# Optimization experiments

Measured on AMD Instinct MI355X. Metric: run time of the kernel, lower is better.

## Reference

```python
import jax, jax.numpy as jnp
import numpy as np

B, G, C = 32, 512, 768
BG = B * G
H = 12              # MHA heads
MID, H1, N1 = 12, 6, 128   # Attention1 mid dim, heads, fixed block size
AD = 16             # adapter bottleneck
FF = 4 * C
NCLUST = 2048       # 3d grid cells
GRID = 196
D1 = B * GRID       # 1d scatter dim_size
NVIEW = 6
SCALE_FACTOR = 0.5
COEF_PRO = 0.3
EPS = 1e-5


def layernorm(x, g, b):
    m = x.mean(-1, keepdims=True)
    v = x.var(-1, keepdims=True)
    return (x - m) / jnp.sqrt(v + EPS) * g + b


def quick_gelu(x):
    return x * jax.nn.sigmoid(1.702 * x)


def bn_gelu(x, g, b):
    # BatchNorm1d in training mode (batch statistics, biased var) + exact GELU
    m = x.mean(0)
    v = x.var(0)
    y = (x - m) / jnp.sqrt(v + EPS) * g + b
    return jax.nn.gelu(y, approximate=False)


def seg_max_mean(feat, idx, nseg):
    # segment_csr(sorted feat, ptr) == segment reduce over cluster ids; empty segments -> 0
    cnt = jax.ops.segment_sum(jnp.ones((feat.shape[0], 1), feat.dtype), idx, nseg)
    smax = jnp.where(cnt > 0, jax.ops.segment_max(feat, idx, nseg), 0.0)
    smean = jax.ops.segment_sum(feat, idx, nseg) / jnp.maximum(cnt, 1.0)
    return smax, smean


def setup_inputs() -> dict:
    key = jax.random.key(0)
    ks = iter(jax.random.split(key, 40))
    r = lambda shape, s=0.02: jax.random.normal(next(ks), shape, jnp.float32) * s
    return {
        "x": jax.random.normal(next(ks), (B, G + 1, C), jnp.float32),
        "ln1_g": jnp.ones((C,)), "ln1_b": jnp.zeros((C,)),
        "ln2_g": jnp.ones((C,)), "ln2_b": jnp.zeros((C,)),
        "Wqkv": r((3 * C, C)), "bqkv": jnp.zeros((3 * C,)),
        "Wo": r((C, C)), "bo": jnp.zeros((C,)),
        "Wfc": r((FF, C)), "bfc": jnp.zeros((FF,)),
        "Wproj": r((C, FF)), "bproj": jnp.zeros((C,)),
        "Wa1": r((AD, C)), "ba1": jnp.zeros((AD,)),
        "Wa2": r((C, AD)), "ba2": jnp.zeros((C,)),
        "bn3d_g": jnp.ones((C,)), "bn3d_b": jnp.zeros((C,)),
        "bn1d_g": jnp.ones((NVIEW, C)), "bn1d_b": jnp.zeros((NVIEW, C)),
        "n3_g": jnp.ones((NVIEW, C)), "n3_b": jnp.zeros((NVIEW, C)),
        "a1_qkv_w": r((NVIEW, 3 * MID, C)), "a1_qkv_b": jnp.zeros((NVIEW, 3 * MID)),
        "a1_proj_w": r((NVIEW, C, MID)), "a1_proj_b": jnp.zeros((NVIEW, C)),
        "cluster": jax.random.randint(next(ks), (BG,), 0, NCLUST),
        "flat_grid_index": jax.random.randint(next(ks), (NVIEW, BG), 0, D1),
        "mask": jax.random.randint(next(ks), (NVIEW, BG // N1, N1, N1), 0, 2).astype(bool),
    }


def reference(x, ln1_g, ln1_b, ln2_g, ln2_b, Wqkv, bqkv, Wo, bo, Wfc, bfc,
              Wproj, bproj, Wa1, ba1, Wa2, ba2, bn3d_g, bn3d_b, bn1d_g, bn1d_b,
              n3_g, n3_b, a1_qkv_w, a1_qkv_b, a1_proj_w, a1_proj_b,
              cluster, flat_grid_index, mask):
    hd = C // H
    # --- multi-head self-attention over tokens + residual ---
    y = layernorm(x, ln1_g, ln1_b)
    qkv = y @ Wqkv.T + bqkv                          # [B, S, 3C]
    q, k, v = jnp.split(qkv, 3, axis=-1)
    heads = lambda t: t.reshape(B, G + 1, H, hd).transpose(0, 2, 1, 3)
    q, k, v = heads(q), heads(k), heads(v)
    attn = jax.nn.softmax(jnp.einsum('bhqd,bhkd->bhqk', q, k) / jnp.sqrt(jnp.float32(hd)), axis=-1)
    o = jnp.einsum('bhqk,bhkd->bhqd', attn, v).transpose(0, 2, 1, 3).reshape(B, G + 1, C)
    x = x + o @ Wo.T + bo
    # --- MLP (QuickGELU) + scaled adapter ---
    y = layernorm(x, ln2_g, ln2_b)
    x_ffn = quick_gelu(y @ Wfc.T + bfc) @ Wproj.T + bproj
    adapt = quick_gelu(x_ffn @ Wa1.T + ba1) @ Wa2.T + ba2
    x = x + x_ffn + SCALE_FACTOR * adapt
    cls_x = x[:, :1]
    xt = x[:, 1:]                                    # [B, G, C]
    feat = xt.reshape(BG, C)
    # --- 3d cluster pooling: segment max+mean -> BN+GELU -> gather back ---
    fmax, fmean = seg_max_mean(feat, cluster, NCLUST)
    x_3d = bn_gelu(fmax + fmean, bn3d_g, bn3d_b)[cluster].reshape(B, G, C)
    # --- per-view local masked attention + 1d grid scatter pooling (vmapped) ---
    def view_branch(n3g, n3b, qkvw, qkvb, projw, projb, bng, bnb, idx, msk):
        z = layernorm(feat, n3g, n3b)
        qkv1 = (z @ qkvw.T + qkvb).reshape(BG // N1, N1, 3, H1, MID // H1).transpose(2, 0, 3, 1, 4)
        q1, k1, v1 = qkv1[0], qkv1[1], qkv1[2]       # [Bn, H1, N1, hd1]
        a = jnp.einsum('bhqd,bhkd->bhqk', q1, k1) * (MID ** -0.5)
        a = a + jnp.where(msk, -100000.0, 0.0)[:, None]  # mask broadcast over heads
        a = jax.nn.softmax(a, axis=-1)
        o1 = jnp.einsum('bhqk,bhkd->bhqd', a, v1).transpose(0, 2, 1, 3).reshape(BG, MID)
        flat = o1 @ projw.T + projb + feat
        smax, smean = seg_max_mean(flat, idx, D1)
        return bn_gelu(smax + smean, bng, bnb)[idx].reshape(B, G, C)
    pos = jax.vmap(view_branch)(n3_g, n3_b, a1_qkv_w, a1_qkv_b, a1_proj_w, a1_proj_b,
                                bn1d_g, bn1d_b, flat_grid_index, mask)   # [6, B, G, C]
    # --- cosine-similarity-weighted fusion of the 6 views against x_3d ---
    def cossim(a, b):
        na = jnp.maximum(jnp.linalg.norm(a, axis=-1), 1e-8)
        nb = jnp.maximum(jnp.linalg.norm(b, axis=-1), 1e-8)
        return (a * b).sum(-1) / (na * nb)
    sims = (jax.vmap(lambda p: cossim(p, x_3d))(pos) + 1.0) / 2.0        # [6, B, G]
    sims = sims / sims.sum(0, keepdims=True)
    x_sup = (pos * sims[..., None]).sum(0)                               # [B, G, C]
    xt = xt + COEF_PRO * x_sup
    return jnp.concatenate([cls_x, xt], axis=1)
```

## Files before the change

kernel.cpp:

```cpp
#include <hip/hip_runtime.h>
#include <hip/hip_bf16.h>
#include <math.h>

typedef unsigned int u32;
typedef __hip_bfloat16 bf16;
typedef __attribute__((ext_vector_type(8))) short bh8;
typedef __attribute__((ext_vector_type(4))) float fx4;
typedef __attribute__((ext_vector_type(2))) unsigned int u32x2;
typedef __attribute__((ext_vector_type(4))) unsigned int u32x4;

#define CDIM   768
#define BATCH  32
#define SEQ    513
#define NT     (BATCH*SEQ)
#define NR     16384
#define NHEAD  12
#define HD     64
#define FFDIM  3072
#define NCLUST 2048
#define D1SEG  6272
#define NVIEW  6
#define MIDD   12
#define H1N    6
#define N1V    128
#define NB1    128
#define CHROWS 8208

#define A_FS      ((size_t)0)
#define B_FS      ((size_t)6303744)
#define X1_FS     ((size_t)25214976)
#define AH_FS     ((size_t)31518720)
#define D_FS      ((size_t)31781376)
#define DTOT_FS   9640064
#define X3D_FS    ((size_t)(D_FS + DTOT_FS))
#define BNV_FS    (X3D_FS + 1572864)
#define STATM_FS  (BNV_FS + 14450688)
#define STATR_FS  (STATM_FS + 768)
#define DI_CNT    (D_FS)
#define DI_BASE   (D_FS + 6272)
#define DI_CUR    (D_FS + 12544)
#define DI_ORD    (D_FS + 18816)
#define DW_FS     (D_FS + 40960)
#define DWV_FS    (D_FS + 3600000)

__device__ inline float b2f(bf16 v){ return __bfloat162float(v); }
__device__ inline float ldv(const float* p, size_t i){ return p[i]; }
__device__ inline float ldv(const bf16*  p, size_t i){ return __bfloat162float(p[i]); }
__device__ inline void  stv(float* p, size_t i, float v){ p[i] = v; }
__device__ inline void  stv(bf16*  p, size_t i, float v){ p[i] = __float2bfloat16(v); }
__device__ inline short f2bs(float f){ bf16 h = __float2bfloat16(f); return *(short*)&h; }
__device__ inline void gload_lds16(const bf16* g, short* l){
    __builtin_amdgcn_global_load_lds((const __attribute__((address_space(1))) void*)g,
                                     (__attribute__((address_space(3))) void*)l, 16, 0, 0);
}
__device__ inline u32x2 ds_tr16(unsigned a){
    u32x2 d;
    asm volatile("ds_read_b64_tr_b16 %0, %1" : "=v"(d) : "v"(a));
    return d;
}
__device__ inline unsigned cvtpk_bf16(float lo, float hi){
    unsigned r;
    asm("v_cvt_pk_bf16_f32 %0, %1, %2" : "=v"(r) : "v"(lo), "v"(hi));
    return r;
}


__global__ __launch_bounds__(256) void k_zero(float* p, int n){
    for (int i = blockIdx.x*256 + threadIdx.x; i < n; i += gridDim.x*256) p[i] = 0.0f;
}

__global__ __launch_bounds__(256) void k_f2b5(const float* __restrict__ a0, bf16* __restrict__ b0, int n0,
                                              const float* __restrict__ a1, bf16* __restrict__ b1, int n1,
                                              const float* __restrict__ a2, bf16* __restrict__ b2, int n2,
                                              const float* __restrict__ a3, bf16* __restrict__ b3, int n3,
                                              const float* __restrict__ a4, bf16* __restrict__ b4, int n4){
    int i0 = blockIdx.x*256 + threadIdx.x, st = gridDim.x*256;
    for (int i=i0; i<n0; i+=st) b0[i] = __float2bfloat16(a0[i]);
    for (int i=i0; i<n1; i+=st) b1[i] = __float2bfloat16(a1[i]);
    for (int i=i0; i<n2; i+=st) b2[i] = __float2bfloat16(a2[i]);
    for (int i=i0; i<n3; i+=st) b3[i] = __float2bfloat16(a3[i]);
    for (int i=i0; i<n4; i+=st) b4[i] = __float2bfloat16(a4[i]);
}

template<typename TI>
__global__ __launch_bounds__(256) void k_ln(const TI* __restrict__ in, bf16* __restrict__ out,
                                            const float* __restrict__ g, const float* __restrict__ b){
    int i = blockIdx.x;
    int tid = threadIdx.x;
    const TI* r = in + (size_t)i*CDIM;
    float v0 = ldv(r,(size_t)tid), v1 = ldv(r,(size_t)tid+256), v2 = ldv(r,(size_t)tid+512);
    float s  = v0+v1+v2;
    float s2 = v0*v0+v1*v1+v2*v2;
    __shared__ float t1[4], t2[4];
    #pragma unroll
    for (int o=32;o;o>>=1){ s += __shfl_down(s,o,64); s2 += __shfl_down(s2,o,64); }
    int lane = tid & 63, wid = tid >> 6;
    if (!lane){ t1[wid]=s; t2[wid]=s2; }
    __syncthreads();
    float S  = t1[0]+t1[1]+t1[2]+t1[3];
    float S2 = t2[0]+t2[1]+t2[2]+t2[3];
    float m  = S * (1.0f/CDIM);
    float var = S2 * (1.0f/CDIM) - m*m;
    float rstd = rsqrtf(var + 1e-5f);
    bf16* o_ = out + (size_t)i*CDIM;
    stv(o_,(size_t)tid,     (v0-m)*rstd*g[tid]     + b[tid]);
    stv(o_,(size_t)tid+256, (v1-m)*rstd*g[tid+256] + b[tid+256]);
    stv(o_,(size_t)tid+512, (v2-m)*rstd*g[tid+512] + b[tid+512]);
}

__global__ __launch_bounds__(256) void k_lnn(const float* __restrict__ in, bf16* __restrict__ out){
    int i = blockIdx.x;
    size_t ri = (size_t)(i + (i>>9) + 1);
    int tid = threadIdx.x;
    const float* r = in + ri*CDIM;
    float v0 = r[tid], v1 = r[tid+256], v2 = r[tid+512];
    float s  = v0+v1+v2;
    float s2 = v0*v0+v1*v1+v2*v2;
    __shared__ float t1[4], t2[4];
    #pragma unroll
    for (int o=32;o;o>>=1){ s += __shfl_down(s,o,64); s2 += __shfl_down(s2,o,64); }
    int lane = tid & 63, wid = tid >> 6;
    if (!lane){ t1[wid]=s; t2[wid]=s2; }
    __syncthreads();
    float S  = t1[0]+t1[1]+t1[2]+t1[3];
    float S2 = t2[0]+t2[1]+t2[2]+t2[3];
    float m  = S * (1.0f/CDIM);
    float var = S2 * (1.0f/CDIM) - m*m;
    float rstd = rsqrtf(var + 1e-5f);
    bf16* o_ = out + (size_t)i*CDIM;
    stv(o_,(size_t)tid,     (v0-m)*rstd);
    stv(o_,(size_t)tid+256, (v1-m)*rstd);
    stv(o_,(size_t)tid+512, (v2-m)*rstd);
}

__global__ __launch_bounds__(256) void k_foldw(const float* __restrict__ aqw, const float* __restrict__ aqb,
                                               const float* __restrict__ n3g, const float* __restrict__ n3b,
                                               bf16* __restrict__ Wv, float* __restrict__ bv){
    int row = blockIdx.x;
    int v = row/36;
    const float* w = aqw + (size_t)row*768;
    const float* g = n3g + v*768;
    const float* b = n3b + v*768;
    int tid = threadIdx.x;
    float s = 0.0f;
    #pragma unroll
    for (int j=tid; j<768; j+=256){
        float wv = w[j];
        Wv[(size_t)row*768 + j] = __float2bfloat16(wv*g[j]);
        s += wv*b[j];
    }
    __shared__ float t1[4];
    #pragma unroll
    for (int o=32;o;o>>=1) s += __shfl_down(s,o,64);
    int lane = tid & 63, wid = tid >> 6;
    if (!lane) t1[wid]=s;
    __syncthreads();
    if (tid==0) bv[row] = aqb[row] + t1[0]+t1[1]+t1[2]+t1[3];
}

template<typename TO, int ACT, int RES>
__global__ __launch_bounds__(256) void k_gemm_mfma(const bf16* __restrict__ A, const bf16* __restrict__ W,
                                                   const float* __restrict__ bias, const float* __restrict__ res,
                                                   TO* __restrict__ out, int M, int N, int K){
    __shared__ short As[3][128*32];
    __shared__ short Ws[3][128*32];
    int nbx = (N + 127) >> 7;
    int nwg = gridDim.x;
    int orig = blockIdx.x;
    int xcd = orig & 7, sl = orig >> 3;
    int q8 = nwg >> 3, r8 = nwg & 7;
    int wg = (xcd < r8 ? xcd*(q8+1) : r8*(q8+1) + (xcd - r8)*q8) + sl;
    int by = wg / nbx;
    int bm = by*128, bn = (wg - by*nbx)*128;
    int tid = threadIdx.x, wid = tid>>6, lane = tid&63, quad = lane>>4, l16 = lane&15;
    int wr = (wid>>1)*64, wc = (wid&1)*64;
    fx4 acc[4][4];
    #pragma unroll
    for (int i=0;i<4;i++)
        #pragma unroll
        for (int j=0;j<4;j++) acc[i][j] = (fx4){0.f,0.f,0.f,0.f};
    int lrow = lane>>2;
    int gchunk = (lane&3) ^ ((lane>>3)&3);
    int r0a0 = wid*32 + lrow,  r0a1 = wid*32 + 16 + lrow;
    int ra0 = bm + r0a0; if (ra0 > M-1) ra0 = M-1;
    int ra1 = bm + r0a1; if (ra1 > M-1) ra1 = M-1;
    int rw0 = bn + r0a0; if (rw0 > N-1) rw0 = N-1;
    int rw1 = bn + r0a1; if (rw1 > N-1) rw1 = N-1;
    const bf16* pa0 = A + (size_t)ra0*K + gchunk*8;
    const bf16* pa1 = A + (size_t)ra1*K + gchunk*8;
    const bf16* pw0 = W + (size_t)rw0*K + gchunk*8;
    const bf16* pw1 = W + (size_t)rw1*K + gchunk*8;
    int sL0 = (wid*32)*32;
    int sL1 = (wid*32 + 16)*32;
    int slotx = (l16>>1)&3;
    int nt = K >> 5;
    #define STAGE4(bsel, t) do { int _k0 = (t) << 5;               \
        gload_lds16(pa0 + _k0, &As[(bsel)][sL0]);                  \
        gload_lds16(pa1 + _k0, &As[(bsel)][sL1]);                  \
        gload_lds16(pw0 + _k0, &Ws[(bsel)][sL0]);                  \
        gload_lds16(pw1 + _k0, &Ws[(bsel)][sL1]); } while(0)
    STAGE4(0, 0);
    STAGE4(1, 1);
    int cur = 0;
    for (int t = 0; t < nt; ++t){
        if (t + 1 < nt) asm volatile("s_waitcnt vmcnt(4)" ::: "memory");
        else            asm volatile("s_waitcnt vmcnt(0)" ::: "memory");
        __builtin_amdgcn_s_barrier();
        __builtin_amdgcn_sched_barrier(0);
        if (t + 2 < nt){
            int nb = cur + 2; if (nb >= 3) nb -= 3;
            STAGE4(nb, t + 2);
        }
        const short* Ab = &As[cur][0];
        const short* Wb = &Ws[cur][0];
        bh8 af[4], bf_[4];
        int sa = (quad ^ slotx)*8;
        #pragma unroll
        for (int i=0;i<4;i++) af[i]  = *(const bh8*)&Ab[(wr + i*16 + l16)*32 + sa];
        #pragma unroll
        for (int j=0;j<4;j++) bf_[j] = *(const bh8*)&Wb[(wc + j*16 + l16)*32 + sa];
        #pragma unroll
        for (int i=0;i<4;i++)
            #pragma unroll
            for (int j=0;j<4;j++)
                acc[i][j] = __builtin_amdgcn_mfma_f32_16x16x32_bf16(af[i], bf_[j], acc[i][j], 0,0,0);
        cur += 1; if (cur == 3) cur = 0;
    }
    #undef STAGE4
    #pragma unroll
    for (int i=0;i<4;i++){
        #pragma unroll
        for (int r=0;r<4;r++){
            int row = bm + wr + i*16 + quad*4 + r;
            if (row >= M) continue;
            #pragma unroll
            for (int j=0;j<4;j++){
                int col = bn + wc + j*16 + l16;
                if (col >= N) continue;
                float v = acc[i][j][r] + bias[col];
                if (ACT == 1) v = v / (1.0f + __expf(-1.702f*v));
                if (RES) v += res[(size_t)row*N + col];
                stv(out, (size_t)row*N + col, v);
            }
        }
    }
}

#define KSTR 72
__global__ __launch_bounds__(256) void k_attn_mfma(const bf16* __restrict__ qkv, bf16* __restrict__ obuf){
    __shared__ short Ks[2][64*KSTR];
    __shared__ short Vs[2][64*KSTR];
    __shared__ short Ps[4*16*KSTR];
    int id = blockIdx.x;
    int qt = (id>>3) % 9;
    int bh = (id&7) + ((id/72)<<3);
    int h = bh % NHEAD, b = bh / NHEAD;
    int tid = threadIdx.x, wid = tid>>6, lane = tid&63, quad = lane>>4, l16 = lane&15;
    size_t base = (size_t)b*SEQ*2304;
    int q_own = qt*64 + wid*16 + l16;
    int q_cl  = q_own > 512 ? 512 : q_own;
    const bf16* qrow = qkv + base + (size_t)q_cl*2304 + h*HD;
    bh8 qa0 = *(const bh8*)(qrow + quad*8);
    bh8 qa1 = *(const bh8*)(qrow + 32 + quad*8);
    {
        union { bh8 v; short s[8]; } u0, u1;
        u0.v = qa0; u1.v = qa1;
        #pragma unroll
        for (int j=0;j<8;j++){
            bf16 a = *(bf16*)&u0.s[j]; u0.s[j] = f2bs(0.125f*b2f(a));
            bf16 c = *(bf16*)&u1.s[j]; u1.s[j] = f2bs(0.125f*b2f(c));
        }
        qa0 = u0.v; qa1 = u1.v;
    }
    fx4 o[4];
    #pragma unroll
    for (int d=0; d<4; d++) o[d] = (fx4){0.f,0.f,0.f,0.f};
    float mrow = -1e30f, lrow = 0.f;
    int srow = tid>>2, d0 = (tid&3)*16;
    int s_st = (srow>>2)*4 + (tid&3);
    int vsb  = (s_st ^ ((srow>>3)<<1))*KSTR + (srow&3)*16;
    short* pw = &Ps[(wid*16 + l16)*KSTR];
    const short* prd0 = &Ps[(wid*16+l16)*KSTR + quad*8];
    const short* prd1 = &Ps[(wid*16+l16)*KSTR + 32 + quad*8];
    unsigned vls = (unsigned)(size_t)(__attribute__((address_space(3))) short*)&Vs[0][0] + 2u*l16;
    #define TRA(vb,hf,c,dt) ((vb) + 144u*(unsigned)(((32*(hf) + 8*quad + 4*(c) + (dt)) ^ (8*(hf) + 2*quad))))
    bh8 kv0, kv1, vv0, vv1;
    {
        const bf16* krow = qkv + base + 768 + (size_t)srow*2304 + h*HD + d0;
        kv0 = *(const bh8*)(krow);
        kv1 = *(const bh8*)(krow + 8);
        vv0 = *(const bh8*)(krow + 768);
        vv1 = *(const bh8*)(krow + 776);
    }
    int p = 0;
    for (int kt=0; kt<9; kt++){
        short* KsP = &Ks[p][0];
        short* VsP = &Vs[p][0];
        *(bh8*)&KsP[srow*KSTR + d0]     = kv0;
        *(bh8*)&KsP[srow*KSTR + d0 + 8] = kv1;
        *(bh8*)&VsP[vsb]     = vv0;
        *(bh8*)&VsP[vsb + 8] = vv1;
        __syncthreads();
        if (kt < 8){
            int kg = (kt+1)*64 + srow; if (kg > 512) kg = 512;
            const bf16* krow = qkv + base + 768 + (size_t)kg*2304 + h*HD + d0;
            kv0 = *(const bh8*)(krow);
            kv1 = *(const bh8*)(krow + 8);
            vv0 = *(const bh8*)(krow + 768);
            vv1 = *(const bh8*)(krow + 776);
        }
        unsigned vb = vls + 9216u*(unsigned)p;
        fx4 s[4];
        __builtin_amdgcn_s_setprio(1);
        #pragma unroll
        for (int nt=0; nt<4; nt++){
            bh8 kb0 = *(const bh8*)&KsP[(nt*16+l16)*KSTR + quad*8];
            bh8 kb1 = *(const bh8*)&KsP[(nt*16+l16)*KSTR + 32 + quad*8];
            fx4 a = (fx4){0.f,0.f,0.f,0.f};
            a = __builtin_amdgcn_mfma_f32_16x16x32_bf16(kb0, qa0, a, 0,0,0);
            a = __builtin_amdgcn_mfma_f32_16x16x32_bf16(kb1, qa1, a, 0,0,0);
            s[nt] = a;
        }
        __builtin_amdgcn_s_setprio(0);
        u32x2 tv[16];
        #pragma unroll
        for (int dt=0; dt<4; dt++){
            tv[dt*4+0] = ds_tr16(TRA(vb,0,0,dt));
            tv[dt*4+1] = ds_tr16(TRA(vb,0,1,dt));
            tv[dt*4+2] = ds_tr16(TRA(vb,1,0,dt));
            tv[dt*4+3] = ds_tr16(TRA(vb,1,1,dt));
        }
        if (kt == 8){
            #pragma unroll
            for (int nt=0; nt<4; nt++)
                #pragma unroll
                for (int r=0;r<4;r++){
                    bool ok = (nt==0) && (r==0) && (quad==0);
                    s[nt][r] = ok ? s[nt][r] : -1e30f;
                }
        }
        float ml = s[0][0];
        #pragma unroll
        for (int nt=0; nt<4; nt++)
            #pragma unroll
            for (int r=0;r<4;r++) if (nt|r) ml = fmaxf(ml, s[nt][r]);
        ml = fmaxf(ml, __shfl_xor(ml, 16, 64));
        ml = fmaxf(ml, __shfl_xor(ml, 32, 64));
        if (__any(ml > mrow)){
            float mn = fmaxf(mrow, ml);
            float al = __expf(mrow - mn);
            mrow = mn;
            lrow *= al;
            float alr[4];
            #pragma unroll
            for (int r=0;r<4;r++) alr[r] = __shfl(al, quad*4 + r, 16);
            #pragma unroll
            for (int d=0; d<4; d++)
                #pragma unroll
                for (int r=0;r<4;r++) o[d][r] *= alr[r];
        }
        float ps = 0.f;
        #pragma unroll
        for (int nt=0; nt<4; nt++)
            #pragma unroll
            for (int r=0;r<4;r++){
                float pp = __expf(s[nt][r] - mrow);
                s[nt][r] = pp;
                ps += pp;
            }
        ps += __shfl_xor(ps, 16, 64);
        ps += __shfl_xor(ps, 32, 64);
        lrow += ps;
        #pragma unroll
        for (int nt=0; nt<4; nt++){
            u32x2 w;
            w[0] = cvtpk_bf16(s[nt][0], s[nt][1]);
            w[1] = cvtpk_bf16(s[nt][2], s[nt][3]);
            *(u32x2*)&pw[nt*16 + quad*4] = w;
        }
        bh8 pa0 = *(const bh8*)prd0;
        bh8 pa1 = *(const bh8*)prd1;
        asm volatile("s_waitcnt lgkmcnt(0)" ::: "memory");
        __builtin_amdgcn_sched_barrier(0);
        __builtin_amdgcn_s_setprio(1);
        #pragma unroll
        for (int dt=0; dt<4; dt++){
            union { u32x4 u; bh8 h; } v0, v1;
            v0.u = (u32x4){tv[dt*4+0][0], tv[dt*4+0][1], tv[dt*4+1][0], tv[dt*4+1][1]};
            v1.u = (u32x4){tv[dt*4+2][0], tv[dt*4+2][1], tv[dt*4+3][0], tv[dt*4+3][1]};
            o[dt] = __builtin_amdgcn_mfma_f32_16x16x32_bf16(pa0, v0.h, o[dt], 0,0,0);
            o[dt] = __builtin_amdgcn_mfma_f32_16x16x32_bf16(pa1, v1.h, o[dt], 0,0,0);
        }
        __builtin_amdgcn_s_setprio(0);
        p ^= 1;
    }
    #undef TRA
    float linv[4];
    #pragma unroll
    for (int r=0;r<4;r++) linv[r] = 1.0f / __shfl(lrow, quad*4 + r, 16);
    #pragma unroll
    for (int r=0;r<4;r++){
        int q = qt*64 + wid*16 + quad*4 + r;
        if (q < SEQ){
            size_t ob = ((size_t)(b*SEQ+q))*CDIM + h*HD;
            #pragma unroll
            for (int dt=0; dt<4; dt++)
                obuf[ob + dt*16 + l16] = __float2bfloat16(o[dt][r]*linv[r]);
        }
    }
}

__global__ __launch_bounds__(256) void k_comb(const bf16* __restrict__ x1, const bf16* __restrict__ xffn,
                                              const float* __restrict__ ah, const float* __restrict__ Wa2,
                                              const float* __restrict__ ba2, float* __restrict__ x2){
    int i = blockIdx.x; int tid = threadIdx.x;
    __shared__ float ar[16];
    if (tid < 16) ar[tid] = ah[(size_t)i*16 + tid];
    __syncthreads();
    for (int c=tid; c<CDIM; c+=256){
        const float* w = Wa2 + (size_t)c*16;
        float a = ba2[c];
        #pragma unroll
        for (int mm=0; mm<16; mm++) a += ar[mm]*w[mm];
        size_t o = (size_t)i*CDIM + c;
        x2[o] = b2f(x1[o]) + b2f(xffn[o]) + 0.5f*a;
    }
}

__global__ __launch_bounds__(256) void k_icount(const int* __restrict__ idx, int* __restrict__ cnt, int n){
    int i = blockIdx.x*256 + threadIdx.x;
    if (i < n) atomicAdd(&cnt[idx[i]], 1);
}

__global__ __launch_bounds__(256) void k_iscan(const int* __restrict__ cnt, int* __restrict__ base,
                                               int* __restrict__ cur, int nseg){
    __shared__ int part[256], off[256];
    int t = threadIdx.x;
    int chunk = (nseg + 255) >> 8;
    int j0 = t*chunk, j1 = j0 + chunk; if (j1 > nseg) j1 = nseg;
    int s = 0;
    for (int j=j0; j<j1; j++) s += cnt[j];
    part[t] = s; __syncthreads();
    if (t == 0){ int acc=0; for (int i=0;i<256;i++){ off[i]=acc; acc+=part[i]; } }
    __syncthreads();
    int acc = off[t];
    for (int j=j0; j<j1; j++){ base[j]=acc; cur[j]=acc; acc+=cnt[j]; }
}

__global__ __launch_bounds__(256) void k_iscatter(const int* __restrict__ idx, int* __restrict__ cur,
                                                  int* __restrict__ order, int n){
    int i = blockIdx.x*256 + threadIdx.x;
    if (i < n){
        int pos = atomicAdd(&cur[idx[i]], 1);
        order[pos] = i;
    }
}

__global__ __launch_bounds__(256) void k_icount6(const int* __restrict__ fgi, int* __restrict__ cnt){
    int g = blockIdx.x*256 + threadIdx.x;
    int v = g >> 14;
    atomicAdd(&cnt[v*D1SEG + fgi[g]], 1);
}

__global__ __launch_bounds__(256) void k_iscan6(const int* __restrict__ cnt, int* __restrict__ base,
                                                int* __restrict__ cur){
    __shared__ int part[256], off[256];
    int v = blockIdx.x;
    const int* c = cnt + v*D1SEG;
    int* bs = base + v*D1SEG;
    int* cu = cur + v*D1SEG;
    int t = threadIdx.x;
    int chunk = (D1SEG + 255) >> 8;
    int j0 = t*chunk, j1 = j0 + chunk; if (j1 > D1SEG) j1 = D1SEG;
    int s = 0;
    for (int j=j0; j<j1; j++) s += c[j];
    part[t] = s; __syncthreads();
    if (t == 0){ int acc=0; for (int i=0;i<256;i++){ off[i]=acc; acc+=part[i]; } }
    __syncthreads();
    int acc = off[t];
    for (int j=j0; j<j1; j++){ bs[j]=acc; cu[j]=acc; acc+=c[j]; }
}

__global__ __launch_bounds__(256) void k_iscatter6(const int* __restrict__ fgi, int* __restrict__ cur,
                                                   int* __restrict__ order){
    int g = blockIdx.x*256 + threadIdx.x;
    int v = g >> 14;
    int pos = atomicAdd(&cur[v*D1SEG + fgi[g]], 1);
    order[(size_t)v*NR + pos] = g & (NR-1);
}

__global__ __launch_bounds__(256) void k_gather_seg(const float* __restrict__ outx, const int* __restrict__ basep,
                                                    const int* __restrict__ cntp, const int* __restrict__ order,
                                                    float* __restrict__ dst){
    int sg = blockIdx.x; int tid = threadIdx.x;
    int n = cntp[sg], b0 = basep[sg];
    float mx[3] = {-1e30f,-1e30f,-1e30f};
    float sm[3] = {0.f,0.f,0.f};
    for (int r=0; r<n; r++){
        int i = order[b0+r];
        size_t rb = (size_t)(i + (i>>9) + 1)*CDIM;
        #pragma unroll
        for (int j=0;j<3;j++){
            float v = outx[rb + tid + j*256];
            mx[j] = fmaxf(mx[j], v); sm[j] += v;
        }
    }
    float den = (float)(n > 1 ? n : 1);
    size_t db = (size_t)sg*CDIM;
    #pragma unroll
    for (int j=0;j<3;j++)
        dst[db + tid + j*256] = (n > 0 ? mx[j] : 0.f) + sm[j]/den;
}

__global__ __launch_bounds__(256) void k_gather_flat(const float* __restrict__ outx, const float* __restrict__ o1v,
                                                     const float* __restrict__ Wp, const float* __restrict__ bp,
                                                     const int* __restrict__ basep, const int* __restrict__ cntp,
                                                     const int* __restrict__ order, float* __restrict__ dst){
    int sg = blockIdx.x; int tid = threadIdx.x;
    int n = cntp[sg], b0 = basep[sg];
    float w[3][MIDD], bb[3];
    #pragma unroll
    for (int j=0;j<3;j++){
        int c = tid + j*256;
        bb[j] = bp[c];
        #pragma unroll
        for (int mm=0;mm<MIDD;mm++) w[j][mm] = Wp[(size_t)c*MIDD + mm];
    }
    float mx[3] = {-1e30f,-1e30f,-1e30f};
    float sm[3] = {0.f,0.f,0.f};
    for (int r=0; r<n; r++){
        int i = order[b0+r];
        const float* orow = o1v + (size_t)i*MIDD;
        float ov[MIDD];
        #pragma unroll
        for (int mm=0;mm<MIDD;mm++) ov[mm] = orow[mm];
        size_t rb = (size_t)(i + (i>>9) + 1)*CDIM;
        #pragma unroll
        for (int j=0;j<3;j++){
            float a = bb[j];
            #pragma unroll
            for (int mm=0;mm<MIDD;mm++) a += ov[mm]*w[j][mm];
            a += outx[rb + tid + j*256];
            mx[j] = fmaxf(mx[j], a); sm[j] += a;
        }
    }
    float den = (float)(n > 1 ? n : 1);
    size_t db = (size_t)sg*CDIM;
    #pragma unroll
    for (int j=0;j<3;j++)
        dst[db + tid + j*256] = (n > 0 ? mx[j] : 0.f) + sm[j]/den;
}

__global__ __launch_bounds__(256) void k_colstats_part(const float* __restrict__ in, int rows,
                                                       float* __restrict__ sumv, float* __restrict__ sumsq){
    int c = blockIdx.x*256 + threadIdx.x;
    if (c >= CDIM) return;
    int chunk = (rows + 31) >> 5;
    int r0 = blockIdx.y*chunk;
    int r1 = r0 + chunk; if (r1 > rows) r1 = rows;
    float s = 0.0f, s2 = 0.0f;
    for (int r=r0; r<r1; r++){
        float v = in[(size_t)r*CDIM + c];
        s += v; s2 += v*v;
    }
    atomicAdd(&sumv[c], s);
    atomicAdd(&sumsq[c], s2);
}

template<typename TO>
__global__ __launch_bounds__(256) void k_bngelu2(const float* __restrict__ in, TO* __restrict__ outp,
                                                 const float* __restrict__ sv, const float* __restrict__ sq,
                                                 const float* __restrict__ g, const float* __restrict__ b,
                                                 int n, float invn){
    int i = blockIdx.x*256 + threadIdx.x;
    if (i >= n) return;
    int c = i - (i/CDIM)*CDIM;
    float m = sv[c]*invn;
    float var = sq[c]*invn - m*m;
    float r = rsqrtf(fmaxf(var, 0.0f) + 1e-5f);
    float y = (in[i]-m)*r*g[c] + b[c];
    stv(outp, (size_t)i, 0.5f*y*(1.0f + erff(y*0.70710678118654752f)));
}

#define MSTR 33
__global__ __launch_bounds__(256) void k_attnv(const float* __restrict__ qkv1a,
                                               const unsigned char* __restrict__ mask,
                                               float* __restrict__ o1all){
    __shared__ float Qs[N1V][13], Ksv[N1V][13], Vsv[N1V][13];
    __shared__ int   Ms[N1V*MSTR];
    int blk = blockIdx.x, v = blockIdx.y;
    int tid = threadIdx.x;
    if (tid < N1V){
        const float4* rp = (const float4*)(qkv1a + (size_t)(blk*N1V + tid)*216 + v*36);
        #pragma unroll
        for (int j=0;j<3;j++){
            float4 q4 = rp[j], k4 = rp[3+j], v4 = rp[6+j];
            Qs[tid][j*4+0]=q4.x; Qs[tid][j*4+1]=q4.y; Qs[tid][j*4+2]=q4.z; Qs[tid][j*4+3]=q4.w;
            Ksv[tid][j*4+0]=k4.x; Ksv[tid][j*4+1]=k4.y; Ksv[tid][j*4+2]=k4.z; Ksv[tid][j*4+3]=k4.w;
            Vsv[tid][j*4+0]=v4.x; Vsv[tid][j*4+1]=v4.y; Vsv[tid][j*4+2]=v4.z; Vsv[tid][j*4+3]=v4.w;
        }
    }
    {
        const int4* mp = (const int4*)(mask + ((size_t)v*NB1 + blk)*N1V*N1V);
        #pragma unroll
        for (int it=0; it<4; it++){
            int e = tid + it*256;
            int4 m4 = mp[e];
            int row = e >> 3, c4 = (e & 7)*4;
            Ms[row*MSTR + c4 + 0] = m4.x;
            Ms[row*MSTR + c4 + 1] = m4.y;
            Ms[row*MSTR + c4 + 2] = m4.z;
            Ms[row*MSTR + c4 + 3] = m4.w;
        }
    }
    __syncthreads();
    int n = tid & 127, hg = tid >> 7;
    const float scale = 0.28867513459481287f;
    #pragma unroll
    for (int hh=0; hh<3; hh++){
        int h = hg*3 + hh;
        float q0 = Qs[n][h*2], q1 = Qs[n][h*2+1];
        float m = -1e30f;
        #pragma unroll 4
        for (int k4=0; k4<32; k4++){
            int mw = Ms[n*MSTR + k4];
            #pragma unroll
            for (int j=0;j<4;j++){
                int k = k4*4 + j;
                float s = (q0*Ksv[k][h*2] + q1*Ksv[k][h*2+1])*scale + (((mw>>(j*8))&0xFF) ? -100000.0f : 0.0f);
                m = fmaxf(m, s);
            }
        }
        float l = 0.f, o0 = 0.f, o1v = 0.f;
        #pragma unroll 4
        for (int k4=0; k4<32; k4++){
            int mw = Ms[n*MSTR + k4];
            #pragma unroll
            for (int j=0;j<4;j++){
                int k = k4*4 + j;
                float s = (q0*Ksv[k][h*2] + q1*Ksv[k][h*2+1])*scale + (((mw>>(j*8))&0xFF) ? -100000.0f : 0.0f);
                float p = __expf(s - m);
                l += p; o0 += p*Vsv[k][h*2]; o1v += p*Vsv[k][h*2+1];
            }
        }
        float inv = 1.0f/l;
        float* orow = o1all + ((size_t)v*NR + blk*N1V + n)*MIDD + h*2;
        orow[0] = o0*inv; orow[1] = o1v*inv;
    }
}

__global__ __launch_bounds__(256) void k_final(float* __restrict__ outx, const float* __restrict__ x3d,
                                               const bf16* __restrict__ bnv, const int* __restrict__ cluster,
                                               const int* __restrict__ fgi){
    int i = blockIdx.x; int tid = threadIdx.x;
    int cl = cluster[i];
    const float* xr = x3d + (size_t)cl*CDIM;
    const bf16* pr[NVIEW];
    #pragma unroll
    for (int v=0; v<NVIEW; v++)
        pr[v] = bnv + ((size_t)v*D1SEG + fgi[(size_t)v*NR + i])*CDIM;
    size_t rb = (size_t)(i + (i>>9) + 1)*CDIM;
    float pv[NVIEW][3], ft[3];
    float dotv[NVIEW] = {0,0,0,0,0,0};
    float np2[NVIEW]  = {0,0,0,0,0,0};
    float nx2 = 0.0f;
    #pragma unroll
    for (int j=0; j<3; j++){
        int c = tid + j*256;
        float xv = xr[c]; nx2 += xv*xv;
        ft[j] = outx[rb + c];
        #pragma unroll
        for (int v=0; v<NVIEW; v++){
            float p = b2f(pr[v][c]); pv[v][j] = p;
            dotv[v] += p*xv; np2[v] += p*p;
        }
    }
    __shared__ float part[4*13];
    __shared__ float ssim[NVIEW];
    float vals[13];
    vals[0] = nx2;
    #pragma unroll
    for (int v=0; v<NVIEW; v++){ vals[1+v] = dotv[v]; vals[7+v] = np2[v]; }
    int lane = tid & 63, wid = tid >> 6;
    #pragma unroll
    for (int k=0; k<13; k++){
        float w = vals[k];
        #pragma unroll
        for (int o=32;o;o>>=1) w += __shfl_down(w,o,64);
        if (!lane) part[wid*13 + k] = w;
    }
    __syncthreads();
    if (tid == 0){
        float tot[13];
        #pragma unroll
        for (int k=0; k<13; k++) tot[k] = part[k] + part[13+k] + part[26+k] + part[39+k];
        float nb = fmaxf(sqrtf(tot[0]), 1e-8f);
        float sv[NVIEW]; float ssumv = 0.0f;
        #pragma unroll
        for (int v=0; v<NVIEW; v++){
            float na = fmaxf(sqrtf(tot[7+v]), 1e-8f);
            float cs = tot[1+v] / (na*nb);
            sv[v] = (cs + 1.0f)*0.5f;
            ssumv += sv[v];
        }
        #pragma unroll
        for (int v=0; v<NVIEW; v++) ssim[v] = sv[v]/ssumv;
    }
    __syncthreads();
    #pragma unroll
    for (int j=0; j<3; j++){
        int c = tid + j*256;
        float xs = 0.0f;
        #pragma unroll
        for (int v=0; v<NVIEW; v++) xs += ssim[v]*pv[v][j];
        outx[rb + c] = ft[j] + 0.3f*xs;
    }
}

extern "C" void kernel_launch(void* const* d_in, const int* in_sizes, int n_in,
                              void* d_out, int out_size, void* d_ws, size_t ws_size,
                              hipStream_t stream){
    const float* x     = (const float*)d_in[0];
    const float* ln1g  = (const float*)d_in[1];
    const float* ln1b  = (const float*)d_in[2];
    const float* ln2g  = (const float*)d_in[3];
    const float* ln2b  = (const float*)d_in[4];
    const float* Wqkv  = (const float*)d_in[5];
    const float* bqkv  = (const float*)d_in[6];
    const float* Wo    = (const float*)d_in[7];
    const float* bo    = (const float*)d_in[8];
    const float* Wfc   = (const float*)d_in[9];
    const float* bfc   = (const float*)d_in[10];
    const float* Wproj = (const float*)d_in[11];
    const float* bproj = (const float*)d_in[12];
    const float* Wa1   = (const float*)d_in[13];
    const float* ba1   = (const float*)d_in[14];
    const float* Wa2   = (const float*)d_in[15];
    const float* ba2   = (const float*)d_in[16];
    const float* bn3dg = (const float*)d_in[17];
    const float* bn3db = (const float*)d_in[18];
    const float* bn1dg = (const float*)d_in[19];
    const float* bn1db = (const float*)d_in[20];
    const float* n3g   = (const float*)d_in[21];
    const float* n3b   = (const float*)d_in[22];
    const float* aqw   = (const float*)d_in[23];
    const float* aqb   = (const float*)d_in[24];
    const float* apw   = (const float*)d_in[25];
    const float* apb   = (const float*)d_in[26];
    const int*   cluster = (const int*)d_in[27];
    const int*   fgi     = (const int*)d_in[28];
    const unsigned char* mask = (const unsigned char*)d_in[29];
    float* out = (float*)d_out;
    float* ws  = (float*)d_ws;

    bf16*  yb    = (bf16*)(ws + A_FS);
    bf16*  qkvb  = (bf16*)(ws + B_FS);
    bf16*  hb    = (bf16*)(ws + B_FS);
    bf16*  xffb  = (bf16*)(ws + B_FS + 12607488);
    float* qkv1a = ws + B_FS;
    float* o1all = ws + B_FS + 3538944;
    float* svs   = ws + B_FS + 4718592;
    bf16*  x1b   = (bf16*)(ws + X1_FS);
    float* ah    = ws + AH_FS;
    int*   icnt  = (int*)(ws + DI_CNT);
    int*   ibase = (int*)(ws + DI_BASE);
    int*   icur  = (int*)(ws + DI_CUR);
    int*   iord  = (int*)(ws + DI_ORD);
    float* x3d   = ws + X3D_FS;
    bf16*  bnv   = (bf16*)(ws + BNV_FS);
    float* statm = ws + STATM_FS;
    float* statr = ws + STATR_FS;
    bf16* WqkvB  = (bf16*)(ws + DW_FS);
    bf16* WoB    = WqkvB + 2304*768;
    bf16* WfcB   = WoB   + 768*768;
    bf16* WprojB = WfcB  + 3072*768;
    bf16* WvB    = (bf16*)(ws + DWV_FS);
    float* bvP   = ws + DWV_FS + 82944;
    bf16* Wa1B   = (bf16*)(ws + DWV_FS + 83200);
    int*   icnt6  = (int*)(ws + AH_FS);
    int*   ibase6 = icnt6 + 6*D1SEG;
    int*   icur6  = ibase6 + 6*D1SEG;
    int*   iord6  = icur6 + 6*D1SEG;
    float* stat6  = (float*)(iord6 + 6*NR);

    k_f2b5<<<2048, 256, 0, stream>>>(Wqkv, WqkvB, 2304*768,  Wo, WoB, 768*768,
                                     Wfc, WfcB, 3072*768,    Wproj, WprojB, 768*3072,
                                     Wa1, Wa1B, 16*768);
    k_foldw<<<216, 256, 0, stream>>>(aqw, aqb, n3g, n3b, WvB, bvP);
    k_ln<float><<<NT, 256, 0, stream>>>(x, yb, ln1g, ln1b);
    k_gemm_mfma<bf16,0,0><<<(2304/128)*((NT+127)/128), 256, 0, stream>>>(yb, WqkvB, bqkv, nullptr, qkvb, NT, 2304, 768);
    k_attn_mfma<<<3456, 256, 0, stream>>>(qkvb, yb);
    k_gemm_mfma<bf16,0,1><<<(768/128)*((NT+127)/128), 256, 0, stream>>>(yb, WoB, bo, x, x1b, NT, 768, 768);
    k_ln<bf16><<<NT, 256, 0, stream>>>(x1b, yb, ln2g, ln2b);
    for (int cch=0; cch<2; cch++){
        const bf16* a2 = yb + (size_t)cch*CHROWS*CDIM;
        bf16* xo = xffb + (size_t)cch*CHROWS*CDIM;
        k_gemm_mfma<bf16,1,0><<<(FFDIM/128)*((CHROWS+127)/128), 256, 0, stream>>>(a2, WfcB, bfc, nullptr, hb, CHROWS, FFDIM, 768);
        k_gemm_mfma<bf16,0,0><<<(768/128)*((CHROWS+127)/128), 256, 0, stream>>>(hb, WprojB, bproj, nullptr, xo, CHROWS, 768, FFDIM);
    }
    k_gemm_mfma<float,1,0><<<1*((NT+127)/128), 256, 0, stream>>>(xffb, Wa1B, ba1, nullptr, ah, NT, 16, 768);
    k_comb<<<NT, 256, 0, stream>>>(x1b, xffb, ah, Wa2, ba2, out);
    k_zero<<<32, 256, 0, stream>>>((float*)icnt, NCLUST);
    k_icount<<<NR/256, 256, 0, stream>>>(cluster, icnt, NR);
    k_iscan<<<1, 256, 0, stream>>>(icnt, ibase, icur, NCLUST);
    k_iscatter<<<NR/256, 256, 0, stream>>>(cluster, icur, iord, NR);
    k_gather_seg<<<NCLUST, 256, 0, stream>>>(out, ibase, icnt, iord, x3d);
    k_zero<<<6, 256, 0, stream>>>(statm, 1536);
    k_colstats_part<<<dim3(3, 32), 256, 0, stream>>>(x3d, NCLUST, statm, statr);
    k_bngelu2<float><<<(NCLUST*CDIM+255)/256, 256, 0, stream>>>(x3d, x3d, statm, statr, bn3dg, bn3db,
                                                                NCLUST*CDIM, 1.0f/NCLUST);
    k_lnn<<<NR, 256, 0, stream>>>(out, yb);
    k_gemm_mfma<float,0,0><<<2*(NR/128), 256, 0, stream>>>(yb, WvB, bvP, nullptr, qkv1a, NR, 216, 768);
    k_attnv<<<dim3(NB1, NVIEW), 256, 0, stream>>>(qkv1a, mask, o1all);
    k_zero<<<(220416+255)/256, 256, 0, stream>>>((float*)icnt6, 220416);
    k_icount6<<<6*NR/256, 256, 0, stream>>>(fgi, icnt6);
    k_iscan6<<<6, 256, 0, stream>>>(icnt6, ibase6, icur6);
    k_iscatter6<<<6*NR/256, 256, 0, stream>>>(fgi, icur6, iord6);
    for (int v=0; v<NVIEW; v++){
        k_gather_flat<<<D1SEG, 256, 0, stream>>>(out, o1all + (size_t)v*NR*MIDD,
                                                 apw + (size_t)v*CDIM*MIDD, apb + (size_t)v*CDIM,
                                                 ibase6 + v*D1SEG, icnt6 + v*D1SEG, iord6 + (size_t)v*NR, svs);
        k_colstats_part<<<dim3(3, 32), 256, 0, stream>>>(svs, D1SEG, stat6 + v*1536, stat6 + v*1536 + 768);
        k_bngelu2<bf16><<<(D1SEG*CDIM+255)/256, 256, 0, stream>>>(svs, bnv + (size_t)v*D1SEG*CDIM,
                                                                  stat6 + v*1536, stat6 + v*1536 + 768,
                                                                  bn1dg + v*CDIM, bn1db + v*CDIM,
                                                                  D1SEG*CDIM, 1.0f/D1SEG);
    }
    k_final<<<NR, 256, 0, stream>>>(out, x3d, bnv, cluster, fgi);
}
```

Measured before the change: 1.592 ms.

## Add 128x256 triple-buffered GEMM with XCD remap, widen column-stats split

Adds a new 512-thread MFMA GEMM kernel that computes 128x256 output tiles, keeps three LDS stages with two tiles loaded ahead, and remaps block IDs so that neighbouring tiles land on the same XCD. The QKV, output-projection, FC and projection GEMMs now use it, aiming for more operand reuse per tile and better latency hiding. Separately, the column-statistics reduction splits rows into 85 chunks instead of 32 so more blocks run in parallel. The larger tiles use more LDS and registers per block, which lowers occupancy and leaves fewer blocks to fill the machine on the narrow N=768 GEMMs.

```diff
diff --git a/kernel.cpp b/kernel.cpp
--- a/kernel.cpp
+++ b/kernel.cpp
@@ -246,6 +246,91 @@
     }
 }
 
+template<typename TO, int ACT, int RES>
+__global__ __launch_bounds__(512) void k_gemm_mfma2(const bf16* __restrict__ A, const bf16* __restrict__ W,
+                                                    const float* __restrict__ bias, const float* __restrict__ res,
+                                                    TO* __restrict__ out, int M, int N, int K){
+    __shared__ short As[3][128*32];
+    __shared__ short Ws[3][256*32];
+    int nbx = (N + 255) >> 8;
+    int nwg = gridDim.x;
+    int orig = blockIdx.x;
+    int xcd = orig & 7, sl = orig >> 3;
+    int q8 = nwg >> 3, r8 = nwg & 7;
+    int wg = (xcd < r8 ? xcd*(q8+1) : r8*(q8+1) + (xcd - r8)*q8) + sl;
+    int by = wg / nbx;
+    int bm = by*128, bn = (wg - by*nbx)*256;
+    int tid = threadIdx.x, wid = tid>>6, lane = tid&63, quad = lane>>4, l16 = lane&15;
+    int wr = (wid>>2)*64, wc = (wid&3)*64;
+    fx4 acc[4][4];
+    #pragma unroll
+    for (int i=0;i<4;i++)
+        #pragma unroll
+        for (int j=0;j<4;j++) acc[i][j] = (fx4){0.f,0.f,0.f,0.f};
+    int lrow = lane>>2;
+    int gchunk = (lane&3) ^ ((lane>>3)&3);
+    int ra0 = bm + wid*16 + lrow;      if (ra0 > M-1) ra0 = M-1;
+    int rw0 = bn + wid*32 + lrow;      if (rw0 > N-1) rw0 = N-1;
+    int rw1 = bn + wid*32 + 16 + lrow; if (rw1 > N-1) rw1 = N-1;
+    const bf16* pa0 = A + (size_t)ra0*K + gchunk*8;
+    const bf16* pw0 = W + (size_t)rw0*K + gchunk*8;
+    const bf16* pw1 = W + (size_t)rw1*K + gchunk*8;
+    int sA  = (wid*16)*32;
+    int sB0 = (wid*32)*32;
+    int sB1 = (wid*32 + 16)*32;
+    int slotx = (l16>>1)&3;
+    int nt = K >> 5;
+    #define STAGE3(bsel, t) do { int _k0 = (t) << 5;               \
+        gload_lds16(pa0 + _k0, &As[(bsel)][sA]);                   \
+        gload_lds16(pw0 + _k0, &Ws[(bsel)][sB0]);                  \
+        gload_lds16(pw1 + _k0, &Ws[(bsel)][sB1]); } while(0)
+    STAGE3(0, 0);
+    STAGE3(1, 1);
+    int cur = 0;
+    for (int t = 0; t < nt; ++t){
+        if (t + 1 < nt) asm volatile("s_waitcnt vmcnt(3)" ::: "memory");
+        else            asm volatile("s_waitcnt vmcnt(0)" ::: "memory");
+        __builtin_amdgcn_s_barrier();
+        __builtin_amdgcn_sched_barrier(0);
+        if (t + 2 < nt){
+            int nb = cur + 2; if (nb >= 3) nb -= 3;
+            STAGE3(nb, t + 2);
+        }
+        const short* Ab = &As[cur][0];
+        const short* Wb = &Ws[cur][0];
+        bh8 af[4], bf_[4];
+        int sa = (quad ^ slotx)*8;
+        #pragma unroll
+        for (int i=0;i<4;i++) af[i]  = *(const bh8*)&Ab[(wr + i*16 + l16)*32 + sa];
+        #pragma unroll
+        for (int j=0;j<4;j++) bf_[j] = *(const bh8*)&Wb[(wc + j*16 + l16)*32 + sa];
+        #pragma unroll
+        for (int i=0;i<4;i++)
+            #pragma unroll
+            for (int j=0;j<4;j++)
+                acc[i][j] = __builtin_amdgcn_mfma_f32_16x16x32_bf16(af[i], bf_[j], acc[i][j], 0,0,0);
+        cur += 1; if (cur == 3) cur = 0;
+    }
+    #undef STAGE3
+    #pragma unroll
+    for (int i=0;i<4;i++){
+        #pragma unroll
+        for (int r=0;r<4;r++){
+            int row = bm + wr + i*16 + quad*4 + r;
+            if (row >= M) continue;
+            #pragma unroll
+            for (int j=0;j<4;j++){
+                int col = bn + wc + j*16 + l16;
+                if (col >= N) continue;
+                float v = acc[i][j][r] + bias[col];
+                if (ACT == 1) v = v / (1.0f + __expf(-1.702f*v));
+                if (RES) v += res[(size_t)row*N + col];
+                stv(out, (size_t)row*N + col, v);
+            }
+        }
+    }
+}
+
 #define KSTR 72
 __global__ __launch_bounds__(256) void k_attn_mfma(const bf16* __restrict__ qkv, bf16* __restrict__ obuf){
     __shared__ short Ks[2][64*KSTR];
@@ -555,7 +640,7 @@
                                                        float* __restrict__ sumv, float* __restrict__ sumsq){
     int c = blockIdx.x*256 + threadIdx.x;
     if (c >= CDIM) return;
-    int chunk = (rows + 31) >> 5;
+    int chunk = (rows + 84) / 85;
     int r0 = blockIdx.y*chunk;
     int r1 = r0 + chunk; if (r1 > rows) r1 = rows;
     float s = 0.0f, s2 = 0.0f;
@@ -788,15 +873,15 @@
                                      Wa1, Wa1B, 16*768);
     k_foldw<<<216, 256, 0, stream>>>(aqw, aqb, n3g, n3b, WvB, bvP);
     k_ln<float><<<NT, 256, 0, stream>>>(x, yb, ln1g, ln1b);
-    k_gemm_mfma<bf16,0,0><<<(2304/128)*((NT+127)/128), 256, 0, stream>>>(yb, WqkvB, bqkv, nullptr, qkvb, NT, 2304, 768);
+    k_gemm_mfma2<bf16,0,0><<<(2304/256)*((NT+127)/128), 512, 0, stream>>>(yb, WqkvB, bqkv, nullptr, qkvb, NT, 2304, 768);
     k_attn_mfma<<<3456, 256, 0, stream>>>(qkvb, yb);
-    k_gemm_mfma<bf16,0,1><<<(768/128)*((NT+127)/128), 256, 0, stream>>>(yb, WoB, bo, x, x1b, NT, 768, 768);
+    k_gemm_mfma2<bf16,0,1><<<(768/256)*((NT+127)/128), 512, 0, stream>>>(yb, WoB, bo, x, x1b, NT, 768, 768);
     k_ln<bf16><<<NT, 256, 0, stream>>>(x1b, yb, ln2g, ln2b);
     for (int cch=0; cch<2; cch++){
         const bf16* a2 = yb + (size_t)cch*CHROWS*CDIM;
         bf16* xo = xffb + (size_t)cch*CHROWS*CDIM;
-        k_gemm_mfma<bf16,1,0><<<(FFDIM/128)*((CHROWS+127)/128), 256, 0, stream>>>(a2, WfcB, bfc, nullptr, hb, CHROWS, FFDIM, 768);
-        k_gemm_mfma<bf16,0,0><<<(768/128)*((CHROWS+127)/128), 256, 0, stream>>>(hb, WprojB, bproj, nullptr, xo, CHROWS, 768, FFDIM);
+        k_gemm_mfma2<bf16,1,0><<<(FFDIM/256)*((CHROWS+127)/128), 512, 0, stream>>>(a2, WfcB, bfc, nullptr, hb, CHROWS, FFDIM, 768);
+        k_gemm_mfma2<bf16,0,0><<<(768/256)*((CHROWS+127)/128), 512, 0, stream>>>(hb, WprojB, bproj, nullptr, xo, CHROWS, 768, FFDIM);
     }
     k_gemm_mfma<float,1,0><<<1*((NT+127)/128), 256, 0, stream>>>(xffb, Wa1B, ba1, nullptr, ah, NT, 16, 768);
     k_comb<<<NT, 256, 0, stream>>>(x1b, xffb, ah, Wa2, ba2, out);
@@ -806,7 +891,7 @@
     k_iscatter<<<NR/256, 256, 0, stream>>>(cluster, icur, iord, NR);
     k_gather_seg<<<NCLUST, 256, 0, stream>>>(out, ibase, icnt, iord, x3d);
     k_zero<<<6, 256, 0, stream>>>(statm, 1536);
-    k_colstats_part<<<dim3(3, 32), 256, 0, stream>>>(x3d, NCLUST, statm, statr);
+    k_colstats_part<<<dim3(3, 85), 256, 0, stream>>>(x3d, NCLUST, statm, statr);
     k_bngelu2<float><<<(NCLUST*CDIM+255)/256, 256, 0, stream>>>(x3d, x3d, statm, statr, bn3dg, bn3db,
                                                                 NCLUST*CDIM, 1.0f/NCLUST);
     k_lnn<<<NR, 256, 0, stream>>>(out, yb);
@@ -820,7 +905,7 @@
         k_gather_flat<<<D1SEG, 256, 0, stream>>>(out, o1all + (size_t)v*NR*MIDD,
                                                  apw + (size_t)v*CDIM*MIDD, apb + (size_t)v*CDIM,
                                                  ibase6 + v*D1SEG, icnt6 + v*D1SEG, iord6 + (size_t)v*NR, svs);
-        k_colstats_part<<<dim3(3, 32), 256, 0, stream>>>(svs, D1SEG, stat6 + v*1536, stat6 + v*1536 + 768);
+        k_colstats_part<<<dim3(3, 85), 256, 0, stream>>>(svs, D1SEG, stat6 + v*1536, stat6 + v*1536 + 768);
         k_bngelu2<bf16><<<(D1SEG*CDIM+255)/256, 256, 0, stream>>>(svs, bnv + (size_t)v*D1SEG*CDIM,
                                                                   stat6 + v*1536, stat6 + v*1536 + 768,
                                                                   bn1dg + v*CDIM, bn1db + v*CDIM,
```

Result: faster. 1.364 ms (-14.3%).
